# Performance work log

Measured on AMD Instinct MI355X. Metric: run time of the kernel, lower is better.

## Reference

```python
import jax, jax.numpy as jnp
import numpy as np

LN_EPS = 1e-5
MODEL_DIM = 256
HEADS = 4


def layer_norm(x, gamma, beta):
    mu = jnp.mean(x, axis=-1, keepdims=True)
    var = jnp.var(x, axis=-1, keepdims=True)
    return (x - mu) * jax.lax.rsqrt(var + LN_EPS) * gamma + beta


def setup_inputs() -> dict:
    key = jax.random.key(0)
    ks = jax.random.split(key, 4)
    bs, s, d, h = 4, 2048, MODEL_DIM, HEADS
    x = jax.random.normal(ks[0], (bs, s, d), dtype=jnp.float32)
    Wq = jax.random.normal(ks[1], (d, h * d), dtype=jnp.float32) / np.sqrt(d)
    Wk = jax.random.normal(ks[2], (d, h * d), dtype=jnp.float32) / np.sqrt(d)
    Wv = jax.random.normal(ks[3], (h * d, d), dtype=jnp.float32) / np.sqrt(h * d)
    gamma = jnp.ones((d,), dtype=jnp.float32)
    beta = jnp.zeros((d,), dtype=jnp.float32)
    return {"x": x, "Wq": Wq, "Wk": Wk, "Wv": Wv, "gamma": gamma, "beta": beta}


def reference(x, Wq, Wk, Wv, gamma, beta):
    bs, s, d = x.shape
    h = Wq.shape[1] // d
    sqrt_norm = jnp.float32(np.sqrt(d))
    # pre_norm = False -> no input LN
    # NOTE: torch does .view(bs, h, s, d) on the (bs, s, h*d) projection --
    # a raw C-order reinterpretation, reproduced here by jnp.reshape.
    Q = jnp.reshape(x @ Wq, (bs, h, s, d))
    K = jnp.reshape(x @ Wk, (bs, h, s, d))
    scores = jnp.einsum('bhid,bhjd->bhij', Q, K)
    probs = jax.nn.softmax(scores / sqrt_norm, axis=-1)  # (bs, h, s, s)
    # value is the shared raw input x broadcast across heads
    out = jnp.einsum('bhij,bjd->bhid', probs, x)
    out = jnp.transpose(out, (0, 2, 1, 3)).reshape(bs, s, h * d)
    out = out @ Wv + x
    out = layer_norm(out, gamma, beta)  # post-norm
    return out, probs
```

## Files before the change

kernel.cpp:

```cpp
#include <hip/hip_runtime.h>

typedef __bf16 bf16;
typedef __bf16 bf16x8 __attribute__((ext_vector_type(8)));
typedef float f32x4 __attribute__((ext_vector_type(4)));

#define BS 4
#define S 2048
#define D 256
#define H 4
#define HD 1024
#define NROW 8192

__device__ __forceinline__ void load_lds16(const bf16* g, bf16* l) {
    __builtin_amdgcn_global_load_lds(
        (const __attribute__((address_space(1))) void*)g,
        (__attribute__((address_space(3))) void*)l, 16, 0, 0);
}

__global__ void prep_x(const float* __restrict__ x, bf16* __restrict__ x_bf,
                       bf16* __restrict__ xT_bf) {
    int idx = blockIdx.x * 256 + threadIdx.x;
    float v = x[idx];
    x_bf[idx] = (bf16)v;
    int dd = idx & (D - 1);
    int t = idx >> 8;
    int j = t & (S - 1);
    int b = t >> 11;
    xT_bf[(size_t)b * D * S + (size_t)dd * S + j] = (bf16)v;
}

__global__ void prep_w(const float* __restrict__ Wq, const float* __restrict__ Wk,
                       const float* __restrict__ Wv, bf16* __restrict__ WqT,
                       bf16* __restrict__ WkT, bf16* __restrict__ WvT) {
    int idx = blockIdx.x * 256 + threadIdx.x;
    const float SCALE = 0.09016844005556021f;
    int seg = idx >> 18;
    int r = idx & 262143;
    if (seg == 0) {
        int k = r & 255, n = r >> 8;
        WqT[r] = (bf16)(Wq[k * HD + n] * SCALE);
    } else if (seg == 1) {
        int k = r & 255, n = r >> 8;
        WkT[r] = (bf16)(Wk[k * HD + n]);
    } else {
        int k = r & 1023, n = r >> 10;
        WvT[r] = (bf16)(Wv[k * D + n]);
    }
}

__global__ __launch_bounds__(256) void gemm_nt_bf16(
    const bf16* __restrict__ A, const bf16* __restrict__ B0,
    const bf16* __restrict__ B1, bf16* __restrict__ C0, bf16* __restrict__ C1,
    int N, int Kd) {
    const bf16* B = blockIdx.z ? B1 : B0;
    bf16* C = blockIdx.z ? C1 : C0;
    int n0 = blockIdx.x * 64;
    int m0 = blockIdx.y * 64;
    __shared__ __align__(16) bf16 As[64 * 40];
    __shared__ __align__(16) bf16 Bs[64 * 40];
    int t = threadIdx.x, w = t >> 6, l = t & 63;
    int lr = l & 15, lq = l >> 4;
    f32x4 acc[4] = {};
    for (int k0 = 0; k0 < Kd; k0 += 32) {
        int row = t >> 2, cb = (t & 3) * 8;
        bf16x8 va = *(const bf16x8*)&A[(size_t)(m0 + row) * Kd + k0 + cb];
        *(bf16x8*)&As[row * 40 + cb] = va;
        bf16x8 vb = *(const bf16x8*)&B[(size_t)(n0 + row) * Kd + k0 + cb];
        *(bf16x8*)&Bs[row * 40 + cb] = vb;
        __syncthreads();
        bf16x8 af = *(const bf16x8*)&As[(w * 16 + lr) * 40 + lq * 8];
#pragma unroll
        for (int nt = 0; nt < 4; nt++) {
            bf16x8 bfr = *(const bf16x8*)&Bs[(nt * 16 + lr) * 40 + lq * 8];
            acc[nt] = __builtin_amdgcn_mfma_f32_16x16x32_bf16(af, bfr, acc[nt], 0, 0, 0);
        }
        __syncthreads();
    }
#pragma unroll
    for (int nt = 0; nt < 4; nt++)
#pragma unroll
        for (int rr = 0; rr < 4; rr++) {
            int row = m0 + w * 16 + lq * 4 + rr;
            C[(size_t)row * N + n0 + nt * 16 + lr] = (bf16)acc[nt][rr];
        }
}

__global__ __launch_bounds__(256, 3) void attn_fused(
    const bf16* __restrict__ Qbf, const bf16* __restrict__ Kbf,
    const bf16* __restrict__ xT, float* __restrict__ probs,
    bf16* __restrict__ attn) {
    int bh = blockIdx.y, b = bh >> 2, h = bh & 3;
    int t = threadIdx.x, w = t >> 6, l = t & 63;
    int lr = l & 15, lq = l >> 4;
    const bf16* Q = Qbf + (size_t)bh * S * D;
    const bf16* K = Kbf + (size_t)bh * S * D;
    const bf16* xTb = xT + (size_t)b * D * S;
    int ibase = blockIdx.x * 64 + w * 16;

    __shared__ __align__(16) bf16 kbuf[32 * 256];
    __shared__ __align__(16) bf16 xbuf[256 * 32];
    __shared__ __align__(16) bf16 pl[4][16 * 40];

    bf16x8 qf[8];
#pragma unroll
    for (int kf = 0; kf < 8; kf++)
        qf[kf] = *(const bf16x8*)&Q[(size_t)(ibase + lr) * D + kf * 32 + lq * 8];

    int krow_l = (w << 3) + (l >> 5);
    int kc_l = l & 31;
    int xrow_l = (w << 6) + (l >> 2);
    int xc_l = l & 3;

    float lsum[4] = {0.f, 0.f, 0.f, 0.f};
    for (int it = 0; it < 64; it++) {
        int j0 = it << 5;
#pragma unroll
        for (int n = 0; n < 4; n++) {
            int r = krow_l + (n << 1);
            int cg = kc_l ^ (r & 7);
            load_lds16(&K[(size_t)(j0 + r) * D + cg * 8], &kbuf[((w << 3) + (n << 1)) * 256]);
        }
        __syncthreads();
#pragma unroll
        for (int subj = 0; subj < 2; subj++) {
            f32x4 acc = {};
#pragma unroll
            for (int kf = 0; kf < 8; kf++) {
                bf16x8 kfr = *(const bf16x8*)
                    &kbuf[(subj * 16 + lr) * 256 + (((kf * 4 + lq) ^ (lr & 7)) * 8)];
                acc = __builtin_amdgcn_mfma_f32_16x16x32_bf16(qf[kf], kfr, acc, 0, 0, 0);
            }
#pragma unroll
            for (int r = 0; r < 4; r++) lsum[r] += exp2f(acc[r]);
        }
        __syncthreads();
    }
    float li[4];
#pragma unroll
    for (int r = 0; r < 4; r++) {
        float s = lsum[r];
        for (int off = 1; off < 16; off <<= 1) s += __shfl_xor(s, off);
        li[r] = 1.0f / s;
    }

    f32x4 oacc[16] = {};
    float* probb = probs + (size_t)bh * S * S;
    for (int it = 0; it < 64; it++) {
        int j0 = it << 5;
#pragma unroll
        for (int n = 0; n < 4; n++) {
            int r = krow_l + (n << 1);
            int cg = kc_l ^ (r & 7);
            load_lds16(&K[(size_t)(j0 + r) * D + cg * 8], &kbuf[((w << 3) + (n << 1)) * 256]);
        }
#pragma unroll
        for (int n = 0; n < 4; n++) {
            int dd = xrow_l + (n << 4);
            int cg = xc_l ^ (dd & 3);
            load_lds16(&xTb[(size_t)dd * S + j0 + cg * 8], &xbuf[((w << 6) + (n << 4)) * 32]);
        }
        __syncthreads();
#pragma unroll
        for (int subj = 0; subj < 2; subj++) {
            f32x4 acc = {};
#pragma unroll
            for (int kf = 0; kf < 8; kf++) {
                bf16x8 kfr = *(const bf16x8*)
                    &kbuf[(subj * 16 + lr) * 256 + (((kf * 4 + lq) ^ (lr & 7)) * 8)];
                acc = __builtin_amdgcn_mfma_f32_16x16x32_bf16(qf[kf], kfr, acc, 0, 0, 0);
            }
#pragma unroll
            for (int r = 0; r < 4; r++) {
                float p = exp2f(acc[r]) * li[r];
                pl[w][(lq * 4 + r) * 40 + subj * 16 + lr] = (bf16)p;
            }
        }
        bf16x8 pf = *(const bf16x8*)&pl[w][lr * 40 + lq * 8];
        f32x4 p0, p1;
#pragma unroll
        for (int e = 0; e < 4; e++) { p0[e] = (float)pf[e]; p1[e] = (float)pf[e + 4]; }
        float* pp = &probb[(size_t)(ibase + lr) * S + j0 + lq * 8];
        *(f32x4*)pp = p0;
        *(f32x4*)(pp + 4) = p1;
#pragma unroll
        for (int dt = 0; dt < 16; dt++) {
            int dd = dt * 16 + lr;
            bf16x8 xf = *(const bf16x8*)&xbuf[dd * 32 + ((lq ^ (lr & 3)) * 8)];
            oacc[dt] = __builtin_amdgcn_mfma_f32_16x16x32_bf16(pf, xf, oacc[dt], 0, 0, 0);
        }
        __syncthreads();
    }
#pragma unroll
    for (int dt = 0; dt < 16; dt++)
#pragma unroll
        for (int rr = 0; rr < 4; rr++) {
            int row = ibase + lq * 4 + rr;
            attn[((size_t)(b * S + row)) * HD + h * D + dt * 16 + lr] = (bf16)oacc[dt][rr];
        }
}

__global__ __launch_bounds__(256) void out_gemm_ln(
    const bf16* __restrict__ attn, const bf16* __restrict__ WvT,
    const float* __restrict__ x, const float* __restrict__ gamma,
    const float* __restrict__ beta, float* __restrict__ out) {
    int m0 = blockIdx.x * 16;
    int t = threadIdx.x, w = t >> 6, l = t & 63;
    int lr = l & 15, lq = l >> 4;
    int ncol0 = w * 64;
    f32x4 acc[4] = {};
    for (int k0 = 0; k0 < HD; k0 += 32) {
        bf16x8 af = *(const bf16x8*)&attn[(size_t)(m0 + lr) * HD + k0 + lq * 8];
#pragma unroll
        for (int dt = 0; dt < 4; dt++) {
            bf16x8 bfr =
                *(const bf16x8*)&WvT[(size_t)(ncol0 + dt * 16 + lr) * HD + k0 + lq * 8];
            acc[dt] = __builtin_amdgcn_mfma_f32_16x16x32_bf16(af, bfr, acc[dt], 0, 0, 0);
        }
    }
    float sum[4] = {0, 0, 0, 0}, sq[4] = {0, 0, 0, 0};
#pragma unroll
    for (int dt = 0; dt < 4; dt++)
#pragma unroll
        for (int rr = 0; rr < 4; rr++) {
            int row = m0 + lq * 4 + rr;
            float v = acc[dt][rr] + x[(size_t)row * D + ncol0 + dt * 16 + lr];
            acc[dt][rr] = v;
            sum[rr] += v;
            sq[rr] += v * v;
        }
#pragma unroll
    for (int rr = 0; rr < 4; rr++)
        for (int off = 1; off < 16; off <<= 1) {
            sum[rr] += __shfl_xor(sum[rr], off);
            sq[rr] += __shfl_xor(sq[rr], off);
        }
    __shared__ float part[4][16][2];
    if (lr == 0)
#pragma unroll
        for (int rr = 0; rr < 4; rr++) {
            part[w][lq * 4 + rr][0] = sum[rr];
            part[w][lq * 4 + rr][1] = sq[rr];
        }
    __syncthreads();
    float mu[4], rs[4];
#pragma unroll
    for (int rr = 0; rr < 4; rr++) {
        int rowi = lq * 4 + rr;
        float s = part[0][rowi][0] + part[1][rowi][0] + part[2][rowi][0] + part[3][rowi][0];
        float q = part[0][rowi][1] + part[1][rowi][1] + part[2][rowi][1] + part[3][rowi][1];
        mu[rr] = s * (1.0f / 256.0f);
        float var = q * (1.0f / 256.0f) - mu[rr] * mu[rr];
        rs[rr] = rsqrtf(var + 1e-5f);
    }
#pragma unroll
    for (int dt = 0; dt < 4; dt++) {
        int col = ncol0 + dt * 16 + lr;
        float g = gamma[col], be = beta[col];
#pragma unroll
        for (int rr = 0; rr < 4; rr++) {
            float v = (acc[dt][rr] - mu[rr]) * rs[rr] * g + be;
            out[(size_t)(m0 + lq * 4 + rr) * D + col] = v;
        }
    }
}

extern "C" void kernel_launch(void* const* d_in, const int* in_sizes, int n_in,
                              void* d_out, int out_size, void* d_ws, size_t ws_size,
                              hipStream_t stream) {
    const float* x = (const float*)d_in[0];
    const float* Wq = (const float*)d_in[1];
    const float* Wk = (const float*)d_in[2];
    const float* Wv = (const float*)d_in[3];
    const float* gamma = (const float*)d_in[4];
    const float* beta = (const float*)d_in[5];
    float* out = (float*)d_out;
    float* probs = out + (size_t)NROW * D;

    char* ws = (char*)d_ws;
    bf16* x_bf = (bf16*)ws;
    bf16* xT_bf = (bf16*)(ws + 4194304);
    bf16* WqT = (bf16*)(ws + 8388608);
    bf16* WkT = (bf16*)(ws + 8912896);
    bf16* WvT = (bf16*)(ws + 9437184);
    bf16* Qbf = (bf16*)(ws + 9961472);
    bf16* Kbf = (bf16*)(ws + 26738688);
    bf16* attn = (bf16*)(ws + 43515904);

    prep_x<<<8192, 256, 0, stream>>>(x, x_bf, xT_bf);
    prep_w<<<3072, 256, 0, stream>>>(Wq, Wk, Wv, WqT, WkT, WvT);
    gemm_nt_bf16<<<dim3(16, 128, 2), 256, 0, stream>>>(x_bf, WqT, WkT, Qbf, Kbf,
                                                       HD, D);
    attn_fused<<<dim3(32, 16), 256, 0, stream>>>(Qbf, Kbf, xT_bf, probs, attn);
    out_gemm_ln<<<512, 256, 0, stream>>>(attn, WvT, x, gamma, beta, out);
}
```

Before: 520.3 us.

## Double-buffer K and x tiles in attention with prefetch and remapped block order

```diff
diff --git a/kernel.cpp b/kernel.cpp
--- a/kernel.cpp
+++ b/kernel.cpp
@@ -85,20 +85,47 @@
         }
 }
 
-__global__ __launch_bounds__(256, 3) void attn_fused(
+__device__ __forceinline__ void stage_k_tile(const bf16* __restrict__ K,
+                                             bf16* kb, int j0, int w, int l) {
+    int krow = (w << 3) + (l >> 5);
+    int kc = l & 31;
+#pragma unroll
+    for (int n = 0; n < 4; n++) {
+        int r = krow + (n << 1);
+        int cg = kc ^ ((r & 3) | ((r & 1) << 2));
+        load_lds16(&K[(size_t)(j0 + r) * D + cg * 8], &kb[((w << 3) + (n << 1)) * 256]);
+    }
+}
+
+__device__ __forceinline__ void stage_x_tile(const bf16* __restrict__ xTb,
+                                             bf16* xb, int j0, int w, int l) {
+    int xrow = (w << 6) + (l >> 2);
+    int xc = l & 3;
+#pragma unroll
+    for (int n = 0; n < 4; n++) {
+        int dd = xrow + (n << 4);
+        int cg = xc ^ (dd & 3);
+        load_lds16(&xTb[(size_t)dd * S + j0 + cg * 8], &xb[((w << 6) + (n << 4)) * 32]);
+    }
+}
+
+__global__ __launch_bounds__(256, 2) void attn_fused(
     const bf16* __restrict__ Qbf, const bf16* __restrict__ Kbf,
     const bf16* __restrict__ xT, float* __restrict__ probs,
     bf16* __restrict__ attn) {
-    int bh = blockIdx.y, b = bh >> 2, h = bh & 3;
+    int nblk = blockIdx.x;
+    int lb = (nblk & 7) * 64 + (nblk >> 3);
+    int bh = lb >> 5, b = bh >> 2, h = bh & 3;
     int t = threadIdx.x, w = t >> 6, l = t & 63;
     int lr = l & 15, lq = l >> 4;
+    int sw = (lr & 3) | ((lr & 1) << 2);
     const bf16* Q = Qbf + (size_t)bh * S * D;
     const bf16* K = Kbf + (size_t)bh * S * D;
     const bf16* xTb = xT + (size_t)b * D * S;
-    int ibase = blockIdx.x * 64 + w * 16;
-
-    __shared__ __align__(16) bf16 kbuf[32 * 256];
-    __shared__ __align__(16) bf16 xbuf[256 * 32];
+    int ibase = (lb & 31) * 64 + w * 16;
+
+    __shared__ __align__(16) bf16 kbuf[2][32 * 256];
+    __shared__ __align__(16) bf16 xbuf[2][256 * 32];
     __shared__ __align__(16) bf16 pl[4][16 * 40];
 
     bf16x8 qf[8];
@@ -106,34 +133,30 @@
     for (int kf = 0; kf < 8; kf++)
         qf[kf] = *(const bf16x8*)&Q[(size_t)(ibase + lr) * D + kf * 32 + lq * 8];
 
-    int krow_l = (w << 3) + (l >> 5);
-    int kc_l = l & 31;
-    int xrow_l = (w << 6) + (l >> 2);
-    int xc_l = l & 3;
-
     float lsum[4] = {0.f, 0.f, 0.f, 0.f};
+    stage_k_tile(K, kbuf[0], 0, w, l);
     for (int it = 0; it < 64; it++) {
-        int j0 = it << 5;
-#pragma unroll
-        for (int n = 0; n < 4; n++) {
-            int r = krow_l + (n << 1);
-            int cg = kc_l ^ (r & 7);
-            load_lds16(&K[(size_t)(j0 + r) * D + cg * 8], &kbuf[((w << 3) + (n << 1)) * 256]);
-        }
-        __syncthreads();
+        int cur = it & 1;
+        if (it < 63) {
+            stage_k_tile(K, kbuf[cur ^ 1], (it + 1) << 5, w, l);
+            asm volatile("s_waitcnt vmcnt(4)" ::: "memory");
+        } else {
+            asm volatile("s_waitcnt vmcnt(0)" ::: "memory");
+        }
+        __builtin_amdgcn_s_barrier();
 #pragma unroll
         for (int subj = 0; subj < 2; subj++) {
             f32x4 acc = {};
 #pragma unroll
             for (int kf = 0; kf < 8; kf++) {
                 bf16x8 kfr = *(const bf16x8*)
-                    &kbuf[(subj * 16 + lr) * 256 + (((kf * 4 + lq) ^ (lr & 7)) * 8)];
+                    &kbuf[cur][(subj * 16 + lr) * 256 + (((kf * 4 + lq) ^ sw) * 8)];
                 acc = __builtin_amdgcn_mfma_f32_16x16x32_bf16(qf[kf], kfr, acc, 0, 0, 0);
             }
 #pragma unroll
             for (int r = 0; r < 4; r++) lsum[r] += exp2f(acc[r]);
         }
-        __syncthreads();
+        __builtin_amdgcn_s_barrier();
     }
     float li[4];
 #pragma unroll
@@ -145,28 +168,26 @@
 
     f32x4 oacc[16] = {};
     float* probb = probs + (size_t)bh * S * S;
+    stage_k_tile(K, kbuf[0], 0, w, l);
+    stage_x_tile(xTb, xbuf[0], 0, w, l);
     for (int it = 0; it < 64; it++) {
+        int cur = it & 1;
         int j0 = it << 5;
-#pragma unroll
-        for (int n = 0; n < 4; n++) {
-            int r = krow_l + (n << 1);
-            int cg = kc_l ^ (r & 7);
-            load_lds16(&K[(size_t)(j0 + r) * D + cg * 8], &kbuf[((w << 3) + (n << 1)) * 256]);
-        }
-#pragma unroll
-        for (int n = 0; n < 4; n++) {
-            int dd = xrow_l + (n << 4);
-            int cg = xc_l ^ (dd & 3);
-            load_lds16(&xTb[(size_t)dd * S + j0 + cg * 8], &xbuf[((w << 6) + (n << 4)) * 32]);
-        }
-        __syncthreads();
+        if (it < 63) {
+            stage_k_tile(K, kbuf[cur ^ 1], j0 + 32, w, l);
+            stage_x_tile(xTb, xbuf[cur ^ 1], j0 + 32, w, l);
+            asm volatile("s_waitcnt vmcnt(8)" ::: "memory");
+        } else {
+            asm volatile("s_waitcnt vmcnt(0)" ::: "memory");
+        }
+        __builtin_amdgcn_s_barrier();
 #pragma unroll
         for (int subj = 0; subj < 2; subj++) {
             f32x4 acc = {};
 #pragma unroll
             for (int kf = 0; kf < 8; kf++) {
                 bf16x8 kfr = *(const bf16x8*)
-                    &kbuf[(subj * 16 + lr) * 256 + (((kf * 4 + lq) ^ (lr & 7)) * 8)];
+                    &kbuf[cur][(subj * 16 + lr) * 256 + (((kf * 4 + lq) ^ sw) * 8)];
                 acc = __builtin_amdgcn_mfma_f32_16x16x32_bf16(qf[kf], kfr, acc, 0, 0, 0);
             }
 #pragma unroll
@@ -185,10 +206,10 @@
 #pragma unroll
         for (int dt = 0; dt < 16; dt++) {
             int dd = dt * 16 + lr;
-            bf16x8 xf = *(const bf16x8*)&xbuf[dd * 32 + ((lq ^ (lr & 3)) * 8)];
+            bf16x8 xf = *(const bf16x8*)&xbuf[cur][dd * 32 + ((lq ^ (lr & 3)) * 8)];
             oacc[dt] = __builtin_amdgcn_mfma_f32_16x16x32_bf16(pf, xf, oacc[dt], 0, 0, 0);
         }
-        __syncthreads();
+        __builtin_amdgcn_s_barrier();
     }
 #pragma unroll
     for (int dt = 0; dt < 16; dt++)
@@ -290,6 +311,6 @@
     prep_w<<<3072, 256, 0, stream>>>(Wq, Wk, Wv, WqT, WkT, WvT);
     gemm_nt_bf16<<<dim3(16, 128, 2), 256, 0, stream>>>(x_bf, WqT, WkT, Qbf, Kbf,
                                                        HD, D);
-    attn_fused<<<dim3(32, 16), 256, 0, stream>>>(Qbf, Kbf, xT_bf, probs, attn);
+    attn_fused<<<dim3(512), 256, 0, stream>>>(Qbf, Kbf, xT_bf, probs, attn);
     out_gemm_ln<<<512, 256, 0, stream>>>(attn, WvT, x, gamma, beta, out);
 }
```

After: 499.2 us. 4.1% less time.
